# Optimization experiments

Measured on AMD Instinct MI355X. Metric: run time of the kernel, lower is better.

The kernel has to match this reference:

```python
import jax, jax.numpy as jnp
import numpy as np

NUM_HEADS = 16
EMBED_DIM = 1024
HEAD_DIM = EMBED_DIM // NUM_HEADS


def setup_inputs() -> dict:
    key = jax.random.key(0)
    k1, k2, k3, k4, k5 = jax.random.split(key, 5)
    b, s, e = 2, 2048, EMBED_DIM
    x = jax.random.normal(k1, (b, s, e), dtype=jnp.float32)
    # torch Linear: y = x @ W.T + b, W shape (out, in)
    w_qkv = jax.random.normal(k2, (3 * e, e), dtype=jnp.float32) * (1.0 / np.sqrt(e))
    b_qkv = jax.random.normal(k3, (3 * e,), dtype=jnp.float32) * 0.02
    w_out = jax.random.normal(k4, (e, e), dtype=jnp.float32) * (1.0 / np.sqrt(e))
    b_out = jax.random.normal(k5, (e,), dtype=jnp.float32) * 0.02
    return {"x": x, "w_qkv": w_qkv, "b_qkv": b_qkv, "w_out": w_out,
            "b_out": b_out, "causal_mask": 1}


def reference(x, w_qkv, b_qkv, w_out, b_out, causal_mask):
    b, s, e = x.shape
    h, d = NUM_HEADS, HEAD_DIM
    qkv = x @ w_qkv.T + b_qkv                      # (b, s, 3e)
    # rearrange 'b s (three h d) -> b h s d three' -> split as (3, h, d)
    qkv = qkv.reshape(b, s, 3, h, d)
    q = jnp.transpose(qkv[:, :, 0], (0, 2, 1, 3))  # (b, h, s, d)
    k = jnp.transpose(qkv[:, :, 1], (0, 2, 1, 3))
    v = jnp.transpose(qkv[:, :, 2], (0, 2, 1, 3))
    scores = jnp.einsum('bhqd,bhkd->bhqk', q, k)   # (b, h, s, s)
    if causal_mask:
        mask = jnp.triu(jnp.ones((s, s), dtype=bool), 1)
        scores = jnp.where(mask, -jnp.inf, scores)
    scores = scores / np.sqrt(d).astype(np.float32)
    probs = jax.nn.softmax(scores, axis=-1)
    out = jnp.einsum('bhqk,bhkd->bhqd', probs, v)  # (b, h, s, d)
    out = jnp.transpose(out, (0, 2, 1, 3)).reshape(b, s, e)
    return out @ w_out.T + b_out
```

## Files before the change

### kernel.cpp

```cpp
#include <hip/hip_runtime.h>
#include <hip/hip_bf16.h>
#include <stdint.h>

static constexpr int S  = 2048;
static constexpr int NH = 16;
static constexpr int HD = 64;
static constexpr int E  = 1024;
static constexpr int BB = 2;
static constexpr int MR = BB * S;

typedef __attribute__((ext_vector_type(8))) short bf16x8;
typedef __attribute__((ext_vector_type(4))) float f32x4;
typedef __attribute__((ext_vector_type(16))) float f32x16;

__device__ __forceinline__ unsigned short f2bf(float f) {
  union { float f; unsigned u; } v; v.f = f;
  unsigned r = v.u + 0x7fffu + ((v.u >> 16) & 1u);
  return (unsigned short)(r >> 16);
}

__device__ __forceinline__ unsigned cvt_pk_bf16(float lo, float hi) {
  unsigned r;
  asm("v_cvt_pk_bf16_f32 %0, %1, %2" : "=v"(r) : "v"(lo), "v"(hi));
  return r;
}

__device__ __forceinline__ f32x4 mfma16(bf16x8 a, bf16x8 b, f32x4 c) {
  return __builtin_amdgcn_mfma_f32_16x16x32_bf16(a, b, c, 0, 0, 0);
}
__device__ __forceinline__ f32x16 mfma32(bf16x8 a, bf16x8 b, f32x16 c) {
  return __builtin_amdgcn_mfma_f32_32x32x16_bf16(a, b, c, 0, 0, 0);
}

__device__ __forceinline__ void gload_lds16(const void* g, void* l) {
  __builtin_amdgcn_global_load_lds(
      (const __attribute__((address_space(1))) uint32_t*)(uintptr_t)g,
      (__attribute__((address_space(3))) uint32_t*)(uintptr_t)l,
      16, 0, 0);
}

__global__ __launch_bounds__(256) void convert_bf16(
    const float* __restrict__ in, unsigned short* __restrict__ out, int n4) {
  int i = blockIdx.x * blockDim.x + threadIdx.x;
  const int stride = gridDim.x * blockDim.x;
  for (; i < n4; i += stride) {
    float4 v = ((const float4*)in)[i];
    ushort4 o;
    o.x = f2bf(v.x); o.y = f2bf(v.y); o.z = f2bf(v.z); o.w = f2bf(v.w);
    ((ushort4*)out)[i] = o;
  }
}

template <int EPI>
__global__ __launch_bounds__(256) void gemm_bt(
    const unsigned short* __restrict__ A, const unsigned short* __restrict__ W,
    const float* __restrict__ bias,
    void* __restrict__ o0, void* __restrict__ o1, void* __restrict__ o2,
    int M, int N, int K) {
  __shared__ __align__(16) unsigned short As[128 * 32];
  __shared__ __align__(16) unsigned short Bs[128 * 32];
  const int tid  = threadIdx.x;
  const int lane = tid & 63;
  const int wid  = tid >> 6;
  const int wm   = wid >> 1;
  const int wn   = wid & 1;
  const int g    = lane >> 4;
  const int lq   = lane & 15;
  const int row0 = blockIdx.y * 128;
  const int col0 = blockIdx.x * 128;
  const int srow = lane >> 2;
  const int sseg = (lane & 3) * 8;

  f32x4 acc[4][4] = {};

  for (int k0 = 0; k0 < K; k0 += 32) {
    __syncthreads();
#pragma unroll
    for (int cc = 0; cc < 2; ++cc) {
      const int c = wid + cc * 4;
      gload_lds16(A + (size_t)(row0 + c * 16 + srow) * K + k0 + sseg,
                  (char*)As + c * 1024);
      gload_lds16(W + (size_t)(col0 + c * 16 + srow) * K + k0 + sseg,
                  (char*)Bs + c * 1024);
    }
    __syncthreads();
    bf16x8 af[4], bfr[4];
#pragma unroll
    for (int m = 0; m < 4; ++m)
      af[m] = *(const bf16x8*)(As + (wm * 64 + m * 16 + lq) * 32 + g * 8);
#pragma unroll
    for (int n = 0; n < 4; ++n)
      bfr[n] = *(const bf16x8*)(Bs + (wn * 64 + n * 16 + lq) * 32 + g * 8);
#pragma unroll
    for (int m = 0; m < 4; ++m)
#pragma unroll
      for (int n = 0; n < 4; ++n)
        acc[m][n] = mfma16(af[m], bfr[n], acc[m][n]);
  }

  if (EPI == 0) {
    unsigned short* Qb = (unsigned short*)o0;
    unsigned short* Kb = (unsigned short*)o1;
    unsigned short* Vt = (unsigned short*)o2;
#pragma unroll
    for (int m = 0; m < 4; ++m) {
      const int rbase = row0 + wm * 64 + m * 16 + g * 4;
#pragma unroll
      for (int n = 0; n < 4; ++n) {
        const int col = col0 + wn * 64 + n * 16 + lq;
        const float bi = bias[col];
        const int three = col >> 10;
        const int rem = col & 1023;
        const int h = rem >> 6, d = rem & 63;
#pragma unroll
        for (int r = 0; r < 4; ++r) {
          const int row = rbase + r;
          const int bb = row >> 11, ss = row & 2047;
          const unsigned short bv = f2bf(acc[m][n][r] + bi);
          if (three == 0)
            Qb[(((size_t)(bb * NH + h)) * S + ss) * HD + d] = bv;
          else if (three == 1)
            Kb[(((size_t)(bb * NH + h)) * S + ss) * HD + d] = bv;
          else
            Vt[(((size_t)(bb * NH + h)) * HD + d) * S + ss] = bv;
        }
      }
    }
  } else {
    float* Out = (float*)o0;
#pragma unroll
    for (int m = 0; m < 4; ++m) {
      const int rbase = row0 + wm * 64 + m * 16 + g * 4;
#pragma unroll
      for (int n = 0; n < 4; ++n) {
        const int col = col0 + wn * 64 + n * 16 + lq;
        const float bi = bias[col];
#pragma unroll
        for (int r = 0; r < 4; ++r)
          Out[(size_t)(rbase + r) * N + col] = acc[m][n][r] + bi;
      }
    }
  }
}

__global__ __launch_bounds__(256) void attn_fwd2(
    const unsigned short* __restrict__ Qb, const unsigned short* __restrict__ Kb,
    const unsigned short* __restrict__ Vt, unsigned short* __restrict__ Ao,
    const int* __restrict__ causal_p) {
  __shared__ __align__(16) unsigned short Ks[64 * 64];
  __shared__ __align__(16) unsigned short Vs[64 * 64];

  const int tid = threadIdx.x, lane = tid & 63, wid = tid >> 6;
  const int cq = lane & 31;
  const int hi = lane >> 5;
  const int id = blockIdx.x;
  const int swz = (id & 7) * 64 + (id >> 3);
  const int bh = swz >> 4;
  const int qt = 15 - (swz & 15);
  const int causal = *causal_p;
  const size_t base  = (size_t)bh * S * HD;
  const size_t vbase = (size_t)bh * HD * S;
  const int qbase = qt * 128 + wid * 32;
  const float CEXP = 0.125f * 1.44269504f;

  bf16x8 qf[4];
#pragma unroll
  for (int f = 0; f < 4; ++f)
    qf[f] = *(const bf16x8*)(Qb + base + (size_t)(qbase + cq) * HD + f * 16 + hi * 8);

  float mM = -1e30f, lS = 0.f;
  f32x16 o0 = {}, o1 = {};

  const int nkt = causal ? (2 * qt + 2) : (S / 64);
  const int r8 = lane >> 3;
  const int ssl = ((lane & 7) ^ r8) * 8;

  for (int kt = 0; kt < nkt; ++kt) {
    __syncthreads();
#pragma unroll
    for (int cc = 0; cc < 2; ++cc) {
      const int c = wid * 2 + cc;
      gload_lds16(Kb + base + (size_t)(kt * 64 + c * 8 + r8) * HD + ssl,
                  (char*)Ks + c * 1024);
      gload_lds16(Vt + vbase + (size_t)(c * 8 + r8) * S + kt * 64 + ssl,
                  (char*)Vs + c * 1024);
    }
    __syncthreads();

    const bool active = (!causal) || (kt * 64 <= qbase + 31);
    if (active) {
      f32x16 sc0 = {}, sc1 = {};
      const int swb = (cq & 7) << 4;
#pragma unroll
      for (int df = 0; df < 4; ++df) {
        const int colb = (df * 32 + hi * 16) ^ swb;
        bf16x8 k0 = *(const bf16x8*)((const char*)Ks + cq * 128 + colb);
        bf16x8 k1 = *(const bf16x8*)((const char*)Ks + (32 + cq) * 128 + colb);
        sc0 = mfma32(k0, qf[df], sc0);
        sc1 = mfma32(k1, qf[df], sc1);
      }

      const bool diag = causal && (kt * 64 + 63 > qbase);
      if (diag) {
        const int q = qbase + cq;
        const int kb = kt * 64 + 4 * hi;
#pragma unroll
        for (int r = 0; r < 16; ++r) {
          const int kl = (r & 3) + 8 * (r >> 2);
          if (kb + kl > q)      sc0[r] = -1e30f;
          if (kb + 32 + kl > q) sc1[r] = -1e30f;
        }
      }

      float mx = -1e30f;
#pragma unroll
      for (int r = 0; r < 16; ++r) {
        mx = fmaxf(mx, sc0[r]);
        mx = fmaxf(mx, sc1[r]);
      }
      mx = fmaxf(mx, __shfl_xor(mx, 32));
      const float mnew = fmaxf(mM, mx);
      const float alpha = exp2f((mM - mnew) * CEXP);
      mM = mnew;
      float rs = 0.f;
#pragma unroll
      for (int r = 0; r < 16; ++r) {
        sc0[r] = exp2f((sc0[r] - mnew) * CEXP);
        sc1[r] = exp2f((sc1[r] - mnew) * CEXP);
        rs += sc0[r] + sc1[r];
      }
      rs += __shfl_xor(rs, 32);
      lS = lS * alpha + rs;
      o0 *= alpha;
      o1 *= alpha;

      unsigned w[16];
#pragma unroll
      for (int i = 0; i < 8; ++i) {
        w[i]     = cvt_pk_bf16(sc0[2 * i], sc0[2 * i + 1]);
        w[i + 8] = cvt_pk_bf16(sc1[2 * i], sc1[2 * i + 1]);
      }

#pragma unroll
      for (int m = 0; m < 4; ++m) {
        const unsigned a = w[4 * m], b = w[4 * m + 1], c = w[4 * m + 2], d = w[4 * m + 3];
        const unsigned ra = __shfl_xor((int)(hi ? a : c), 32);
        const unsigned rb = __shfl_xor((int)(hi ? b : d), 32);
        union { unsigned u[4]; bf16x8 v; } pf;
        pf.u[0] = hi ? ra : a;
        pf.u[1] = hi ? rb : b;
        pf.u[2] = hi ? c : ra;
        pf.u[3] = hi ? d : rb;
        const int colb = (m * 32 + hi * 16) ^ swb;
        bf16x8 v0 = *(const bf16x8*)((const char*)Vs + cq * 128 + colb);
        bf16x8 v1 = *(const bf16x8*)((const char*)Vs + (32 + cq) * 128 + colb);
        o0 = mfma32(v0, pf.v, o0);
        o1 = mfma32(v1, pf.v, o1);
      }
    }
  }

  const int bb2 = bh >> 4, hh = bh & 15;
  unsigned short* orow = Ao + (((size_t)bb2 * S + (qbase + cq)) * NH + hh) * HD;
  const float inv = 1.0f / lS;
#pragma unroll
  for (int i = 0; i < 4; ++i) {
    ushort4 u0, u1;
    u0.x = f2bf(o0[4 * i + 0] * inv); u0.y = f2bf(o0[4 * i + 1] * inv);
    u0.z = f2bf(o0[4 * i + 2] * inv); u0.w = f2bf(o0[4 * i + 3] * inv);
    u1.x = f2bf(o1[4 * i + 0] * inv); u1.y = f2bf(o1[4 * i + 1] * inv);
    u1.z = f2bf(o1[4 * i + 2] * inv); u1.w = f2bf(o1[4 * i + 3] * inv);
    *(ushort4*)(orow + i * 8 + 4 * hi) = u0;
    *(ushort4*)(orow + 32 + i * 8 + 4 * hi) = u1;
  }
}

extern "C" void kernel_launch(void* const* d_in, const int* in_sizes, int n_in,
                              void* d_out, int out_size, void* d_ws, size_t ws_size,
                              hipStream_t stream) {
  const float* x     = (const float*)d_in[0];
  const float* w_qkv = (const float*)d_in[1];
  const float* b_qkv = (const float*)d_in[2];
  const float* w_out = (const float*)d_in[3];
  const float* b_out = (const float*)d_in[4];
  const int*   causal = (const int*)d_in[5];

  char* ws = (char*)d_ws;
  unsigned short* xb    = (unsigned short*)(ws);
  unsigned short* wqkvb = (unsigned short*)(ws + 8388608);
  unsigned short* wob   = (unsigned short*)(ws + 14680064);
  unsigned short* Qb    = (unsigned short*)(ws + 16777216);
  unsigned short* Kb    = (unsigned short*)(ws + 25165824);
  unsigned short* Vtb   = (unsigned short*)(ws + 33554432);
  unsigned short* attnb = (unsigned short*)(ws + 41943040);

  convert_bf16<<<1024, 256, 0, stream>>>(x, xb, (BB * S * E) / 4);
  convert_bf16<<<1024, 256, 0, stream>>>(w_qkv, wqkvb, (3 * E * E) / 4);
  convert_bf16<<<512, 256, 0, stream>>>(w_out, wob, (E * E) / 4);

  gemm_bt<0><<<dim3(3 * E / 128, MR / 128), 256, 0, stream>>>(
      xb, wqkvb, b_qkv, Qb, Kb, Vtb, MR, 3 * E, E);

  attn_fwd2<<<512, 256, 0, stream>>>(Qb, Kb, Vtb, attnb, causal);

  gemm_bt<1><<<dim3(E / 128, MR / 128), 256, 0, stream>>>(
      attnb, wob, b_out, d_out, nullptr, nullptr, MR, E, E);
}
```

Measured before the change: 258.8 us.

## Double-buffer K/V tiles in attention and fold softmax scale into Q

Rewrites the attention kernel with 64-query blocks of 2 waves (1024 blocks), double-buffered K/V shared-memory tiles where the next tile is prefetched while the current one is computed, and a single barrier per iteration. The softmax scale times log2(e) is now applied to Q in the QKV GEMM epilogue, so the inner loop avoids the per-score multiply. It also adds lazy max rescaling (only when the max grows by more than 8), ILP-split reductions and s_setprio around the MFMAs. Costs are double the LDS per block, smaller blocks with less K/V reuse, and Q rounded to bf16 after scaling.

```diff
diff --git a/kernel.cpp b/kernel.cpp
--- a/kernel.cpp
+++ b/kernel.cpp
@@ -102,6 +102,7 @@
     unsigned short* Qb = (unsigned short*)o0;
     unsigned short* Kb = (unsigned short*)o1;
     unsigned short* Vt = (unsigned short*)o2;
+    const float qsc = 0.125f * 1.44269504f;
 #pragma unroll
     for (int m = 0; m < 4; ++m) {
       const int rbase = row0 + wm * 64 + m * 16 + g * 4;
@@ -116,7 +117,9 @@
         for (int r = 0; r < 4; ++r) {
           const int row = rbase + r;
           const int bb = row >> 11, ss = row & 2047;
-          const unsigned short bv = f2bf(acc[m][n][r] + bi);
+          float val = acc[m][n][r] + bi;
+          if (three == 0) val *= qsc;
+          const unsigned short bv = f2bf(val);
           if (three == 0)
             Qb[(((size_t)(bb * NH + h)) * S + ss) * HD + d] = bv;
           else if (three == 1)
@@ -143,125 +146,150 @@
   }
 }
 
-__global__ __launch_bounds__(256) void attn_fwd2(
+__global__ __launch_bounds__(128) void attn_fwd3(
     const unsigned short* __restrict__ Qb, const unsigned short* __restrict__ Kb,
     const unsigned short* __restrict__ Vt, unsigned short* __restrict__ Ao,
     const int* __restrict__ causal_p) {
-  __shared__ __align__(16) unsigned short Ks[64 * 64];
-  __shared__ __align__(16) unsigned short Vs[64 * 64];
+  __shared__ __align__(16) unsigned short Ks[2][64 * 64];
+  __shared__ __align__(16) unsigned short Vs[2][64 * 64];
 
   const int tid = threadIdx.x, lane = tid & 63, wid = tid >> 6;
   const int cq = lane & 31;
   const int hi = lane >> 5;
   const int id = blockIdx.x;
-  const int swz = (id & 7) * 64 + (id >> 3);
-  const int bh = swz >> 4;
-  const int qt = 15 - (swz & 15);
+  const int swz = (id & 7) * 128 + (id >> 3);
+  const int bh = swz >> 5;
+  const int qt = 31 - (swz & 31);
   const int causal = *causal_p;
   const size_t base  = (size_t)bh * S * HD;
   const size_t vbase = (size_t)bh * HD * S;
-  const int qbase = qt * 128 + wid * 32;
-  const float CEXP = 0.125f * 1.44269504f;
+  const int qw = qt * 64 + wid * 32;
 
   bf16x8 qf[4];
 #pragma unroll
   for (int f = 0; f < 4; ++f)
-    qf[f] = *(const bf16x8*)(Qb + base + (size_t)(qbase + cq) * HD + f * 16 + hi * 8);
+    qf[f] = *(const bf16x8*)(Qb + base + (size_t)(qw + cq) * HD + f * 16 + hi * 8);
 
   float mM = -1e30f, lS = 0.f;
   f32x16 o0 = {}, o1 = {};
 
-  const int nkt = causal ? (2 * qt + 2) : (S / 64);
   const int r8 = lane >> 3;
   const int ssl = ((lane & 7) ^ r8) * 8;
+  const int nkt = causal ? (qt + 1) : (S / 64);
+
+#define STAGE(bufi, kt)                                                        \
+  {                                                                            \
+    _Pragma("unroll")                                                          \
+    for (int i = 0; i < 4; ++i) {                                              \
+      const int c = wid * 4 + i;                                               \
+      gload_lds16(Kb + base + (size_t)((kt) * 64 + c * 8 + r8) * HD + ssl,     \
+                  (char*)Ks[bufi] + c * 1024);                                 \
+      gload_lds16(Vt + vbase + (size_t)(c * 8 + r8) * S + (kt) * 64 + ssl,     \
+                  (char*)Vs[bufi] + c * 1024);                                 \
+    }                                                                          \
+  }
+
+  STAGE(0, 0)
+  int buf = 0;
 
   for (int kt = 0; kt < nkt; ++kt) {
-    __syncthreads();
-#pragma unroll
-    for (int cc = 0; cc < 2; ++cc) {
-      const int c = wid * 2 + cc;
-      gload_lds16(Kb + base + (size_t)(kt * 64 + c * 8 + r8) * HD + ssl,
-                  (char*)Ks + c * 1024);
-      gload_lds16(Vt + vbase + (size_t)(c * 8 + r8) * S + kt * 64 + ssl,
-                  (char*)Vs + c * 1024);
-    }
-    __syncthreads();
-
-    const bool active = (!causal) || (kt * 64 <= qbase + 31);
-    if (active) {
-      f32x16 sc0 = {}, sc1 = {};
-      const int swb = (cq & 7) << 4;
-#pragma unroll
-      for (int df = 0; df < 4; ++df) {
-        const int colb = (df * 32 + hi * 16) ^ swb;
-        bf16x8 k0 = *(const bf16x8*)((const char*)Ks + cq * 128 + colb);
-        bf16x8 k1 = *(const bf16x8*)((const char*)Ks + (32 + cq) * 128 + colb);
-        sc0 = mfma32(k0, qf[df], sc0);
-        sc1 = mfma32(k1, qf[df], sc1);
+    asm volatile("s_waitcnt vmcnt(0)" ::: "memory");
+    __builtin_amdgcn_s_barrier();
+    if (kt + 1 < nkt) STAGE(buf ^ 1, kt + 1)
+
+    const char* Kp = (const char*)Ks[buf];
+    const char* Vp = (const char*)Vs[buf];
+    const int swb = (cq & 7) << 4;
+
+    f32x16 sc0 = {}, sc1 = {};
+    __builtin_amdgcn_s_setprio(1);
+#pragma unroll
+    for (int df = 0; df < 4; ++df) {
+      const int colb = (df * 32 + hi * 16) ^ swb;
+      bf16x8 k0 = *(const bf16x8*)(Kp + cq * 128 + colb);
+      bf16x8 k1 = *(const bf16x8*)(Kp + (32 + cq) * 128 + colb);
+      sc0 = mfma32(k0, qf[df], sc0);
+      sc1 = mfma32(k1, qf[df], sc1);
+    }
+    __builtin_amdgcn_s_setprio(0);
+
+    if (causal && kt == nkt - 1) {
+      const int q = qw + cq;
+      const int kb = kt * 64 + 4 * hi;
+#pragma unroll
+      for (int r = 0; r < 16; ++r) {
+        const int kl = (r & 3) + 8 * (r >> 2);
+        if (kb + kl > q)      sc0[r] = -1e30f;
+        if (kb + 32 + kl > q) sc1[r] = -1e30f;
       }
-
-      const bool diag = causal && (kt * 64 + 63 > qbase);
-      if (diag) {
-        const int q = qbase + cq;
-        const int kb = kt * 64 + 4 * hi;
-#pragma unroll
-        for (int r = 0; r < 16; ++r) {
-          const int kl = (r & 3) + 8 * (r >> 2);
-          if (kb + kl > q)      sc0[r] = -1e30f;
-          if (kb + 32 + kl > q) sc1[r] = -1e30f;
-        }
-      }
-
-      float mx = -1e30f;
-#pragma unroll
-      for (int r = 0; r < 16; ++r) {
-        mx = fmaxf(mx, sc0[r]);
-        mx = fmaxf(mx, sc1[r]);
-      }
-      mx = fmaxf(mx, __shfl_xor(mx, 32));
+    }
+
+    float m0 = fmaxf(sc0[0], sc1[0]), m1 = fmaxf(sc0[1], sc1[1]);
+    float m2 = fmaxf(sc0[2], sc1[2]), m3 = fmaxf(sc0[3], sc1[3]);
+#pragma unroll
+    for (int r = 4; r < 16; r += 4) {
+      m0 = fmaxf(m0, fmaxf(sc0[r],     sc1[r]));
+      m1 = fmaxf(m1, fmaxf(sc0[r + 1], sc1[r + 1]));
+      m2 = fmaxf(m2, fmaxf(sc0[r + 2], sc1[r + 2]));
+      m3 = fmaxf(m3, fmaxf(sc0[r + 3], sc1[r + 3]));
+    }
+    float mx = fmaxf(fmaxf(m0, m1), fmaxf(m2, m3));
+    mx = fmaxf(mx, __shfl_xor(mx, 32));
+
+    if (__any(mx > mM + 8.0f)) {
       const float mnew = fmaxf(mM, mx);
-      const float alpha = exp2f((mM - mnew) * CEXP);
+      const float al = exp2f(mM - mnew);
       mM = mnew;
-      float rs = 0.f;
-#pragma unroll
-      for (int r = 0; r < 16; ++r) {
-        sc0[r] = exp2f((sc0[r] - mnew) * CEXP);
-        sc1[r] = exp2f((sc1[r] - mnew) * CEXP);
-        rs += sc0[r] + sc1[r];
-      }
-      rs += __shfl_xor(rs, 32);
-      lS = lS * alpha + rs;
-      o0 *= alpha;
-      o1 *= alpha;
-
-      unsigned w[16];
-#pragma unroll
-      for (int i = 0; i < 8; ++i) {
-        w[i]     = cvt_pk_bf16(sc0[2 * i], sc0[2 * i + 1]);
-        w[i + 8] = cvt_pk_bf16(sc1[2 * i], sc1[2 * i + 1]);
-      }
-
-#pragma unroll
-      for (int m = 0; m < 4; ++m) {
-        const unsigned a = w[4 * m], b = w[4 * m + 1], c = w[4 * m + 2], d = w[4 * m + 3];
-        const unsigned ra = __shfl_xor((int)(hi ? a : c), 32);
-        const unsigned rb = __shfl_xor((int)(hi ? b : d), 32);
-        union { unsigned u[4]; bf16x8 v; } pf;
-        pf.u[0] = hi ? ra : a;
-        pf.u[1] = hi ? rb : b;
-        pf.u[2] = hi ? c : ra;
-        pf.u[3] = hi ? d : rb;
-        const int colb = (m * 32 + hi * 16) ^ swb;
-        bf16x8 v0 = *(const bf16x8*)((const char*)Vs + cq * 128 + colb);
-        bf16x8 v1 = *(const bf16x8*)((const char*)Vs + (32 + cq) * 128 + colb);
-        o0 = mfma32(v0, pf.v, o0);
-        o1 = mfma32(v1, pf.v, o1);
-      }
-    }
-  }
+      lS *= al; o0 *= al; o1 *= al;
+    }
+
+    float r0 = 0.f, r1 = 0.f, r2 = 0.f, r3 = 0.f;
+#pragma unroll
+    for (int r = 0; r < 16; r += 4) {
+      sc0[r]     = exp2f(sc0[r]     - mM); sc1[r]     = exp2f(sc1[r]     - mM);
+      sc0[r + 1] = exp2f(sc0[r + 1] - mM); sc1[r + 1] = exp2f(sc1[r + 1] - mM);
+      sc0[r + 2] = exp2f(sc0[r + 2] - mM); sc1[r + 2] = exp2f(sc1[r + 2] - mM);
+      sc0[r + 3] = exp2f(sc0[r + 3] - mM); sc1[r + 3] = exp2f(sc1[r + 3] - mM);
+      r0 += sc0[r]     + sc1[r];
+      r1 += sc0[r + 1] + sc1[r + 1];
+      r2 += sc0[r + 2] + sc1[r + 2];
+      r3 += sc0[r + 3] + sc1[r + 3];
+    }
+    float rs = (r0 + r1) + (r2 + r3);
+    rs += __shfl_xor(rs, 32);
+    lS += rs;
+
+    unsigned w[16];
+#pragma unroll
+    for (int i = 0; i < 8; ++i) {
+      w[i]     = cvt_pk_bf16(sc0[2 * i], sc0[2 * i + 1]);
+      w[i + 8] = cvt_pk_bf16(sc1[2 * i], sc1[2 * i + 1]);
+    }
+
+#pragma unroll
+    for (int m = 0; m < 4; ++m) {
+      const unsigned a = w[4 * m], b = w[4 * m + 1], c = w[4 * m + 2], d = w[4 * m + 3];
+      const unsigned ra = __shfl_xor((int)(hi ? a : c), 32);
+      const unsigned rb = __shfl_xor((int)(hi ? b : d), 32);
+      union { unsigned u[4]; bf16x8 v; } pf;
+      pf.u[0] = hi ? ra : a;
+      pf.u[1] = hi ? rb : b;
+      pf.u[2] = hi ? c : ra;
+      pf.u[3] = hi ? d : rb;
+      const int colb = (m * 32 + hi * 16) ^ swb;
+      bf16x8 v0 = *(const bf16x8*)(Vp + cq * 128 + colb);
+      bf16x8 v1 = *(const bf16x8*)(Vp + (32 + cq) * 128 + colb);
+      __builtin_amdgcn_s_setprio(1);
+      o0 = mfma32(v0, pf.v, o0);
+      o1 = mfma32(v1, pf.v, o1);
+      __builtin_amdgcn_s_setprio(0);
+    }
+    buf ^= 1;
+  }
+#undef STAGE
 
   const int bb2 = bh >> 4, hh = bh & 15;
-  unsigned short* orow = Ao + (((size_t)bb2 * S + (qbase + cq)) * NH + hh) * HD;
+  unsigned short* orow = Ao + (((size_t)bb2 * S + (qw + cq)) * NH + hh) * HD;
   const float inv = 1.0f / lS;
 #pragma unroll
   for (int i = 0; i < 4; ++i) {
@@ -301,7 +329,7 @@
   gemm_bt<0><<<dim3(3 * E / 128, MR / 128), 256, 0, stream>>>(
       xb, wqkvb, b_qkv, Qb, Kb, Vtb, MR, 3 * E, E);
 
-  attn_fwd2<<<512, 256, 0, stream>>>(Qb, Kb, Vtb, attnb, causal);
+  attn_fwd3<<<1024, 128, 0, stream>>>(Qb, Kb, Vtb, attnb, causal);
 
   gemm_bt<1><<<dim3(E / 128, MR / 128), 256, 0, stream>>>(
       attnb, wob, b_out, d_out, nullptr, nullptr, MR, E, E);
```

Measured after the change: 259.5 us. About the same (+0.3%).
